# Kernel tuning notes

Hardware: AMD Instinct MI355X
Metric: run time of the kernel (lower is better)

The kernel has to match this reference:

```python
import jax, jax.numpy as jnp
import numpy as np

SQ = 1.0 / np.sqrt(2.0)

def _haar_filters():
    dec_lo = np.array([SQ, SQ], np.float32); dec_hi = np.array([-SQ, SQ], np.float32)
    rec_lo = np.array([SQ, SQ], np.float32); rec_hi = np.array([SQ, -SQ], np.float32)
    def bank(lo, hi):
        ks = []
        for fz in (lo, hi):
            for fy in (lo, hi):
                for fx in (lo, hi):
                    ks.append(np.einsum('i,j,k->ijk', fz, fy, fx))
        return jnp.asarray(np.stack(ks, 0))  # [8,2,2,2]
    return bank(dec_lo, dec_hi), bank(rec_lo, rec_hi)

WT_F, IWT_F = _haar_filters()

def dwt3(x):
    # stride-2 2x2x2 cross-correlation == reshape + einsum (kernel size == stride)
    B, C, D, H, W = x.shape
    xr = x.reshape(B, C, D // 2, 2, H // 2, 2, W // 2, 2)
    return jnp.einsum('bcdzhywx,fzyx->bcfdhw', xr, WT_F)  # [B,C,8,D/2,H/2,W/2]

def idwt3(x):
    # conv_transpose3d stride 2 kernel 2: no overlap -> einsum + reshape
    B, C, _, D, H, W = x.shape
    out = jnp.einsum('bcfdhw,fzyx->bcdzhywx', x, IWT_F)
    return out.reshape(B, C, 2 * D, 2 * H, 2 * W)

def dwconv3(x, w, b=None):
    # depthwise 3x3x3 conv, padding SAME (torch padding='same', groups=C)
    y = jax.lax.conv_general_dilated(
        x, w, (1, 1, 1), 'SAME',
        dimension_numbers=('NCDHW', 'OIDHW', 'NCDHW'),
        feature_group_count=x.shape[1])
    if b is not None:
        y = y + b[None, :, None, None, None]
    return y

WT_LEVELS = 2

def setup_inputs() -> dict:
    key = jax.random.key(0)
    ks = jax.random.split(key, 6)
    B, C, D, H, W = 1, 64, 64, 64, 64
    return {
        'x': jax.random.normal(ks[0], (B, C, D, H, W), jnp.float32),
        'base_w': jax.random.normal(ks[1], (C, 1, 3, 3, 3), jnp.float32) * 0.1,
        'base_b': jax.random.normal(ks[2], (C,), jnp.float32) * 0.02,
        'base_scale_w': jnp.ones((1, C, 1, 1, 1), jnp.float32),
        'wconv_w0': jax.random.normal(ks[3], (C * 8, 1, 3, 3, 3), jnp.float32) * 0.1,
        'wconv_w1': jax.random.normal(ks[4], (C * 8, 1, 3, 3, 3), jnp.float32) * 0.1,
        'wscale0': jnp.full((1, C * 8, 1, 1, 1), 0.1, jnp.float32),
        'wscale1': jnp.full((1, C * 8, 1, 1, 1), 0.1, jnp.float32),
        'lambd': jnp.float32(0.05),
    }

def reference(x, base_w, base_b, base_scale_w, wconv_w0, wconv_w1, wscale0, wscale1, lambd):
    wconv_ws = (wconv_w0, wconv_w1)
    wscales = (wscale0, wscale1)
    lls, hfs, shapes = [], [], []
    cur = x
    for i in range(WT_LEVELS):
        shapes.append(cur.shape)
        pd, ph, pw = cur.shape[2] % 2, cur.shape[3] % 2, cur.shape[4] % 2
        if pd or ph or pw:
            cur = jnp.pad(cur, ((0, 0), (0, 0), (0, pd), (0, ph), (0, pw)))
        cx = dwt3(cur)                     # [B,C,8,d,h,w]
        cur = cx[:, :, 0]                  # LL passes to next level
        B, C, _, d, h, w = cx.shape
        t = dwconv3(cx.reshape(B, C * 8, d, h, w), wconv_ws[i])
        t = t.reshape(B, C, 8, d, h, w)
        ll, hf = t[:, :, :1], t[:, :, 1:]
        hf = jnp.sign(hf) * jax.nn.relu(jnp.abs(hf) - lambd)  # soft threshold
        t = jnp.concatenate([ll, hf], axis=2)
        t = (t.reshape(B, C * 8, d, h, w) * wscales[i]).reshape(B, C, 8, d, h, w)
        lls.append(t[:, :, 0]); hfs.append(t[:, :, 1:])
    nxt = jnp.float32(0.0)
    for i in range(WT_LEVELS - 1, -1, -1):
        cll = lls[i] + nxt
        cx = jnp.concatenate([cll[:, :, None], hfs[i]], axis=2)
        nxt = idwt3(cx)
        sh = shapes[i]
        nxt = nxt[:, :, :sh[2], :sh[3], :sh[4]]
    base = dwconv3(x, base_w, base_b) * base_scale_w
    return base + nxt
```

## Files before the change

### kernel.cpp

```cpp
#include <hip/hip_runtime.h>

#define SQ3F 0.35355339059327379f

__device__ __forceinline__ void haar_fwd(const float v[8], float o[8]) {
    float ax[8];
#pragma unroll
    for (int i = 0; i < 4; ++i) {
        float a = v[2 * i], b = v[2 * i + 1];
        ax[2 * i]     = a + b;
        ax[2 * i + 1] = b - a;
    }
    float ay[8];
#pragma unroll
    for (int z = 0; z < 2; ++z)
#pragma unroll
        for (int bx = 0; bx < 2; ++bx) {
            float a = ax[z * 4 + bx], b = ax[z * 4 + 2 + bx];
            ay[z * 4 + bx]     = a + b;
            ay[z * 4 + 2 + bx] = b - a;
        }
#pragma unroll
    for (int j = 0; j < 4; ++j) {
        float a = ay[j], b = ay[4 + j];
        o[j]     = (a + b) * SQ3F;
        o[4 + j] = (b - a) * SQ3F;
    }
}

__device__ __forceinline__ void haar_inv(const float t[8], float o[8]) {
    float az[8];
#pragma unroll
    for (int j = 0; j < 4; ++j) {
        float lo = t[j], hi = t[4 + j];
        az[j]     = lo + hi;
        az[4 + j] = lo - hi;
    }
    float ay[8];
#pragma unroll
    for (int z = 0; z < 2; ++z)
#pragma unroll
        for (int bx = 0; bx < 2; ++bx) {
            float lo = az[z * 4 + bx], hi = az[z * 4 + 2 + bx];
            ay[z * 4 + bx]     = lo + hi;
            ay[z * 4 + 2 + bx] = lo - hi;
        }
#pragma unroll
    for (int i = 0; i < 4; ++i) {
        float lo = ay[2 * i], hi = ay[2 * i + 1];
        o[2 * i]     = (lo + hi) * SQ3F;
        o[2 * i + 1] = (lo - hi) * SQ3F;
    }
}

__global__ __launch_bounds__(512, 4) void fused_l0_k(
    const float* __restrict__ x, const float* __restrict__ wt,
    const float* __restrict__ wscale, const float* __restrict__ lambd_p,
    float* __restrict__ t0, float* __restrict__ ll) {
    __shared__ __align__(16) float pl[8][32][36];
    int bx   = blockIdx.x;
    int slab = bx & 7;
    int c    = bx >> 3;
    int z0   = slab * 4;
    int tid  = threadIdx.x;

    {
        int fi   = tid >> 6;
        int rowi = (tid >> 1) & 31;
        pl[fi][rowi][(tid & 1) * 33] = 0.f;
    }

    int f    = __builtin_amdgcn_readfirstlane(tid >> 6);
    int lane = tid & 63;
    int cty  = lane >> 1;
    int cx0i = (lane & 1) * 16;
    int cc   = c * 8 + f;
    float wv[27];
    const float* wp = wt + cc * 27;
#pragma unroll
    for (int k = 0; k < 27; ++k) wv[k] = wp[k];
    float lam = *lambd_p;
    float sc  = wscale[cc];

    const float* xc = x + ((long)c << 18);

    int y0c = tid >> 5;
    int xx0 = tid & 31;

    float2 ld[2][4];

    auto issue_loads = [&](int p) {
#pragma unroll
        for (int half = 0; half < 2; ++half) {
            int y = y0c + half * 16;
#pragma unroll
            for (int z = 0; z < 2; ++z)
#pragma unroll
                for (int yy = 0; yy < 2; ++yy)
                    ld[half][z * 2 + yy] = *(const float2*)(
                        xc + (((2 * p + z) << 6) + (2 * y + yy)) * 64 + 2 * xx0);
        }
    };
    auto stage_write = [&](int p, bool dolls) {
#pragma unroll
        for (int half = 0; half < 2; ++half) {
            int y = y0c + half * 16;
            float v[8];
            v[0] = ld[half][0].x; v[1] = ld[half][0].y;
            v[2] = ld[half][1].x; v[3] = ld[half][1].y;
            v[4] = ld[half][2].x; v[5] = ld[half][2].y;
            v[6] = ld[half][3].x; v[7] = ld[half][3].y;
            float o[8];
            haar_fwd(v, o);
#pragma unroll
            for (int k = 0; k < 8; ++k) pl[k][y][xx0 + 1] = o[k];
            if (dolls) ll[(c << 15) + (p << 10) + (y << 5) + xx0] = o[0];
        }
    };

    float acc[3][16];
#pragma unroll
    for (int s = 0; s < 3; ++s)
#pragma unroll
        for (int j = 0; j < 16; ++j) acc[s][j] = 0.f;

    {
        int p = z0 - 1;
        if (p >= 0) {
            issue_loads(p);
            stage_write(p, false);
        }
    }
    __syncthreads();

#pragma unroll
    for (int pp = 0; pp < 6; ++pp) {
        int p       = z0 - 1 + pp;
        bool pvalid = (p >= 0) && (p <= 31);
        int pn      = p + 1;
        bool pnv    = (pp < 5) && (pn <= 31);

        if (pnv) issue_loads(pn);

        if (pvalid) {
#pragma unroll
            for (int dy = 0; dy < 3; ++dy) {
                int yy = cty - 1 + dy;
                if ((unsigned)yy < 32u) {
                    float r[18];
                    {
                        const float* rp = &pl[f][yy][cx0i];
                        float4 a0 = *(const float4*)(rp);
                        float4 a1 = *(const float4*)(rp + 4);
                        float4 a2 = *(const float4*)(rp + 8);
                        float4 a3 = *(const float4*)(rp + 12);
                        float2 a4 = *(const float2*)(rp + 16);
                        r[0]  = a0.x; r[1]  = a0.y; r[2]  = a0.z; r[3]  = a0.w;
                        r[4]  = a1.x; r[5]  = a1.y; r[6]  = a1.z; r[7]  = a1.w;
                        r[8]  = a2.x; r[9]  = a2.y; r[10] = a2.z; r[11] = a2.w;
                        r[12] = a3.x; r[13] = a3.y; r[14] = a3.z; r[15] = a3.w;
                        r[16] = a4.x; r[17] = a4.y;
                    }
#pragma unroll
                    for (int dz = 0; dz < 3; ++dz) {
                        int rel = pp - dz;
                        if (rel >= 0 && rel <= 3) {
                            int s = rel % 3;
#pragma unroll
                            for (int dx = 0; dx < 3; ++dx) {
                                float wgt = wv[dz * 9 + dy * 3 + dx];
#pragma unroll
                                for (int j = 0; j < 16; ++j)
                                    acc[s][j] += r[dx + j] * wgt;
                            }
                        }
                    }
                }
            }
        }
        {
            int rel = pp - 2;
            if (rel >= 0 && rel <= 3) {
                int zc = z0 + rel;
                int s  = rel % 3;
                float res[16];
#pragma unroll
                for (int j = 0; j < 16; ++j) {
                    float t = acc[s][j];
                    if (f != 0) {
                        float a = fabsf(t) - lam;
                        t       = a > 0.f ? copysignf(a, t) : 0.f;
                    }
                    res[j]    = t * sc;
                    acc[s][j] = 0.f;
                }
                float* op = t0 + ((long)cc << 15) + (zc << 10) + cty * 32 + cx0i;
#pragma unroll
                for (int q = 0; q < 4; ++q)
                    *(float4*)(op + q * 4) = float4{res[q * 4], res[q * 4 + 1],
                                                    res[q * 4 + 2], res[q * 4 + 3]};
            }
        }
        __syncthreads();
        if (pnv) stage_write(pn, pp < 4);
        __syncthreads();
    }
}

template <int SO>
__global__ __launch_bounds__(256) void dwt3_k(const float* __restrict__ in,
                                              int inChStride,
                                              float* __restrict__ out) {
    constexpr int SI = SO * 2;
    int idx = blockIdx.x * 256 + threadIdx.x;
    int w = idx % SO;
    int h = (idx / SO) % SO;
    int d = (idx / (SO * SO)) % SO;
    int c = idx / (SO * SO * SO);
    const float* ip = in + (long)c * inChStride;
    float v[8];
#pragma unroll
    for (int z = 0; z < 2; ++z)
#pragma unroll
        for (int y = 0; y < 2; ++y) {
            const float2 p =
                *(const float2*)(ip + ((2 * d + z) * SI + (2 * h + y)) * SI + 2 * w);
            v[z * 4 + y * 2]     = p.x;
            v[z * 4 + y * 2 + 1] = p.y;
        }
    float o[8];
    haar_fwd(v, o);
    int s = (d * SO + h) * SO + w;
#pragma unroll
    for (int f = 0; f < 8; ++f) out[(c * 8 + f) * (SO * SO * SO) + s] = o[f];
}

template <int S, int PH>
__device__ __forceinline__ void conv_step(const float* __restrict__ ip, int zo,
                                          int ty, int x0,
                                          const float* __restrict__ wv,
                                          float win[3][3][6], float lam, float sc,
                                          bool hf, float* __restrict__ op) {
    constexpr int sPrev = (PH + 2) % 3;
    constexpr int sCur  = PH;
    constexpr int sNext = (PH + 1) % 3;
    {
        int zz = zo + 1;
        bool zok = zz < S;
        const float* pp = ip + zz * S * S;
#pragma unroll
        for (int dy = 0; dy < 3; ++dy) {
            int yy  = ty - 1 + dy;
            bool yok = zok && ((unsigned)yy < (unsigned)S);
            const float* rp = pp + yy * S;
            win[sNext][dy][0] = (yok && x0 > 0) ? rp[x0 - 1] : 0.f;
            float4 m = yok ? *(const float4*)(rp + x0) : float4{0.f, 0.f, 0.f, 0.f};
            win[sNext][dy][1] = m.x;
            win[sNext][dy][2] = m.y;
            win[sNext][dy][3] = m.z;
            win[sNext][dy][4] = m.w;
            win[sNext][dy][5] = (yok && (x0 + 4 < S)) ? rp[x0 + 4] : 0.f;
        }
    }
    float acc[4] = {0.f, 0.f, 0.f, 0.f};
#pragma unroll
    for (int dz = 0; dz < 3; ++dz) {
        const float(*wp)[6] = (dz == 0) ? win[sPrev] : (dz == 1) ? win[sCur] : win[sNext];
#pragma unroll
        for (int dy = 0; dy < 3; ++dy)
#pragma unroll
            for (int dx = 0; dx < 3; ++dx) {
                float wgt = wv[dz * 9 + dy * 3 + dx];
#pragma unroll
                for (int j = 0; j < 4; ++j) acc[j] += wp[dy][dx + j] * wgt;
            }
    }
    float4 r;
    float* rr = (float*)&r;
#pragma unroll
    for (int j = 0; j < 4; ++j) {
        float t = acc[j];
        if (hf) {
            float a = fabsf(t) - lam;
            t       = a > 0.f ? copysignf(a, t) : 0.f;
        }
        rr[j] = t * sc;
    }
    *(float4*)(op + (zo * S + ty) * S + x0) = r;
}

template <int S, int SLOT>
__device__ __forceinline__ void load_win_plane(const float* __restrict__ ip,
                                               int z, int ty, int x0,
                                               float win[3][3][6]) {
    bool zok = ((unsigned)z < (unsigned)S);
    const float* pp = ip + z * S * S;
#pragma unroll
    for (int dy = 0; dy < 3; ++dy) {
        int yy  = ty - 1 + dy;
        bool yok = zok && ((unsigned)yy < (unsigned)S);
        const float* rp = pp + yy * S;
        win[SLOT][dy][0] = (yok && x0 > 0) ? rp[x0 - 1] : 0.f;
        float4 m = yok ? *(const float4*)(rp + x0) : float4{0.f, 0.f, 0.f, 0.f};
        win[SLOT][dy][1] = m.x;
        win[SLOT][dy][2] = m.y;
        win[SLOT][dy][3] = m.z;
        win[SLOT][dy][4] = m.w;
        win[SLOT][dy][5] = (yok && (x0 + 4 < S)) ? rp[x0 + 4] : 0.f;
    }
}

template <int S, int PH0>
__device__ __forceinline__ void run_chunk(const float* __restrict__ ip, int z0,
                                          int ty, int x0,
                                          const float* __restrict__ wv,
                                          float win[3][3][6], float lam, float sc,
                                          bool hf, float* __restrict__ op) {
    load_win_plane<S, (PH0 + 2) % 3>(ip, z0 - 1, ty, x0, win);
    load_win_plane<S, PH0>(ip, z0, ty, x0, win);
    conv_step<S, PH0>(ip, z0, ty, x0, wv, win, lam, sc, hf, op);
    conv_step<S, (PH0 + 1) % 3>(ip, z0 + 1, ty, x0, wv, win, lam, sc, hf, op);
    conv_step<S, (PH0 + 2) % 3>(ip, z0 + 2, ty, x0, wv, win, lam, sc, hf, op);
    conv_step<S, PH0>(ip, z0 + 3, ty, x0, wv, win, lam, sc, hf, op);
}

template <int S, int CPB>
__global__ __launch_bounds__(256) void dwconv_soft_chunk_k(
    const float* __restrict__ in, const float* __restrict__ wt,
    const float* __restrict__ wscale, const float* __restrict__ lambd_p,
    float* __restrict__ out) {
    constexpr int TX = S / 4;
    int tid = threadIdx.x;
    int tx  = tid % TX;
    int ty  = (tid / TX) % S;
    int cs  = tid / (TX * S);
    int zc  = blockIdx.x & 3;
    int cg  = blockIdx.x >> 2;
    int cc  = cg * CPB + cs;
    const float* ip = in + (long)cc * (S * S * S);
    float* op       = out + (long)cc * (S * S * S);
    float wv[27];
#pragma unroll
    for (int k = 0; k < 27; ++k) wv[k] = wt[cc * 27 + k];
    float lam = *lambd_p;
    float sc  = wscale[cc];
    bool hf   = (cc & 7) != 0;
    int x0    = 4 * tx;

    float win[3][3][6];
    switch (zc) {
        case 0:  run_chunk<S, 0>(ip, 0,  ty, x0, wv, win, lam, sc, hf, op); break;
        case 1:  run_chunk<S, 1>(ip, 4,  ty, x0, wv, win, lam, sc, hf, op); break;
        case 2:  run_chunk<S, 2>(ip, 8,  ty, x0, wv, win, lam, sc, hf, op); break;
        default: run_chunk<S, 0>(ip, 12, ty, x0, wv, win, lam, sc, hf, op); break;
    }
}

__global__ __launch_bounds__(256, 3) void final_k2(
    const float* __restrict__ x, const float* __restrict__ t0,
    const float* __restrict__ t1, const float* __restrict__ bw,
    const float* __restrict__ bb, const float* __restrict__ bscale,
    float* __restrict__ out) {
    __shared__ float xs[18 * 10 * 67];
    int bx = blockIdx.x;
    int c  = bx >> 5;
    int ti = bx & 31;
    int dt = ti >> 3;
    int ht = ti & 7;
    const float* xc = x + ((long)c << 18);
    int zg0 = 16 * dt - 1, yg0 = 8 * ht - 1;
    for (int i = threadIdx.x; i < 18 * 10 * 66; i += 256) {
        int pz = i / 660;
        int r  = i - pz * 660;
        int py = r / 66;
        int px = r - py * 66;
        int zg = zg0 + pz, yg = yg0 + py, xg = px - 1;
        bool ok = ((unsigned)zg < 64u) && ((unsigned)yg < 64u) && ((unsigned)xg < 64u);
        xs[(pz * 10 + py) * 67 + px] = ok ? xc[(zg << 12) + (yg << 6) + xg] : 0.f;
    }
    const float* wp0 = bw + c * 27;
    float wv[27];
#pragma unroll
    for (int k = 0; k < 27; ++k) wv[k] = wp0[k];
    float bias = bb[c], scl = bscale[c];
    __syncthreads();

    int tid = threadIdx.x;
    int wc  = tid & 7;
    int hc  = (tid >> 3) & 3;
    int dc  = tid >> 5;
    int d   = dt * 8 + dc;
    int h   = ht * 4 + hc;
    int w0  = wc * 4;

    float acc[2][2][8];
#pragma unroll
    for (int oz = 0; oz < 2; ++oz)
#pragma unroll
        for (int oy = 0; oy < 2; ++oy)
#pragma unroll
            for (int m = 0; m < 8; ++m) acc[oz][oy][m] = 0.f;

#pragma unroll
    for (int pz = 0; pz < 4; ++pz) {
        float r[4][10];
#pragma unroll
        for (int py = 0; py < 4; ++py)
#pragma unroll
            for (int k = 0; k < 10; ++k)
                r[py][k] = xs[((2 * dc + pz) * 10 + (2 * hc + py)) * 67 + 8 * wc + k];
#pragma unroll
        for (int oz = 0; oz < 2; ++oz) {
            int kz = pz - oz;
            if (kz >= 0 && kz <= 2) {
#pragma unroll
                for (int py = 0; py < 4; ++py)
#pragma unroll
                    for (int oy = 0; oy < 2; ++oy) {
                        int ky = py - oy;
                        if (ky >= 0 && ky <= 2) {
#pragma unroll
                            for (int kx = 0; kx < 3; ++kx) {
                                float wgt = wv[kz * 9 + ky * 3 + kx];
#pragma unroll
                                for (int m = 0; m < 8; ++m)
                                    acc[oz][oy][m] += r[py][m + kx] * wgt;
                            }
                        }
                    }
            }
        }
    }

    int cell0 = (d << 10) + (h << 5) + w0;
    float4 t0v[8];
#pragma unroll
    for (int f = 0; f < 8; ++f)
        t0v[f] = *(const float4*)(t0 + (((long)(c * 8 + f)) << 15) + cell0);
    int s1b = ((d >> 1) * 16 + (h >> 1)) * 16 + (w0 >> 1);
    float2 t1v[8];
#pragma unroll
    for (int f = 0; f < 8; ++f)
        t1v[f] = *(const float2*)(t1 + ((c * 8 + f) << 12) + s1b);

#pragma unroll
    for (int j = 0; j < 4; ++j) {
        int w = w0 + j;
        float tf[8];
#pragma unroll
        for (int f = 0; f < 8; ++f) tf[f] = ((const float*)&t0v[f])[j];
        float add = 0.f;
#pragma unroll
        for (int f = 0; f < 8; ++f) {
            float v  = (j >> 1) ? t1v[f].y : t1v[f].x;
            float sg = 1.f;
            if ((f & 4) && (d & 1)) sg = -sg;
            if ((f & 2) && (h & 1)) sg = -sg;
            if ((f & 1) && (j & 1)) sg = -sg;
            add += sg * v;
        }
        tf[0] += add * SQ3F;
        float contrib[8];
        haar_inv(tf, contrib);
#pragma unroll
        for (int oz = 0; oz < 2; ++oz)
#pragma unroll
            for (int oy = 0; oy < 2; ++oy) {
                float2 rr;
                rr.x = (acc[oz][oy][2 * j] + bias) * scl + contrib[oz * 4 + oy * 2];
                rr.y = (acc[oz][oy][2 * j + 1] + bias) * scl +
                       contrib[oz * 4 + oy * 2 + 1];
                *(float2*)(out + ((long)c << 18) + ((2 * d + oz) << 12) +
                           ((2 * h + oy) << 6) + 2 * w) = rr;
            }
    }
}

extern "C" void kernel_launch(void* const* d_in, const int* in_sizes, int n_in,
                              void* d_out, int out_size, void* d_ws, size_t ws_size,
                              hipStream_t stream) {
    const float* x      = (const float*)d_in[0];
    const float* base_w = (const float*)d_in[1];
    const float* base_b = (const float*)d_in[2];
    const float* base_s = (const float*)d_in[3];
    const float* w0     = (const float*)d_in[4];
    const float* w1     = (const float*)d_in[5];
    const float* ws0    = (const float*)d_in[6];
    const float* ws1    = (const float*)d_in[7];
    const float* lambd  = (const float*)d_in[8];
    float* out = (float*)d_out;

    float* ll  = (float*)d_ws;
    float* t0  = ll + 2097152;
    float* cx1 = t0 + 16777216;
    float* t1  = cx1 + 2097152;

    fused_l0_k<<<512, 512, 0, stream>>>(x, w0, ws0, lambd, t0, ll);
    dwt3_k<16><<<1024, 256, 0, stream>>>(ll, 32768, cx1);
    dwconv_soft_chunk_k<16, 4><<<512, 256, 0, stream>>>(cx1, w1, ws1, lambd, t1);
    final_k2<<<2048, 256, 0, stream>>>(x, t0, t1, base_w, base_b, base_s, out);
}
```

Before: 259.0 us.

## Drop level-0 prefetch pipeline and double threads in final fused kernel

In the fused level-0 kernel, the register-prefetch software pipeline is replaced by a simpler per-plane load of float4s. Each thread now transforms two adjacent Haar cells and stores LL as float2, with one sync on each side. The final kernel moves from 256 to 512 threads per block, halving per-thread output width, and now writes contiguous float4 rows. It also broadcasts the uniform weights with readfirstlane to keep them in scalar registers. The intent is more parallelism, lower register pressure and wider stores, at the cost of losing load/compute overlap in the level-0 kernel and recomputing more halo reads per thread.

```diff
diff --git a/kernel.cpp b/kernel.cpp
--- a/kernel.cpp
+++ b/kernel.cpp
@@ -1,6 +1,10 @@
 #include <hip/hip_runtime.h>
 
 #define SQ3F 0.35355339059327379f
+
+__device__ __forceinline__ float rfl(float v) {
+    return __int_as_float(__builtin_amdgcn_readfirstlane(__float_as_int(v)));
+}
 
 __device__ __forceinline__ void haar_fwd(const float v[8], float o[8]) {
     float ax[8];
@@ -83,64 +87,46 @@
 
     const float* xc = x + ((long)c << 18);
 
-    int y0c = tid >> 5;
-    int xx0 = tid & 31;
-
-    float2 ld[2][4];
-
-    auto issue_loads = [&](int p) {
-#pragma unroll
-        for (int half = 0; half < 2; ++half) {
-            int y = y0c + half * 16;
-#pragma unroll
-            for (int z = 0; z < 2; ++z)
-#pragma unroll
-                for (int yy = 0; yy < 2; ++yy)
-                    ld[half][z * 2 + yy] = *(const float2*)(
-                        xc + (((2 * p + z) << 6) + (2 * y + yy)) * 64 + 2 * xx0);
-        }
-    };
-    auto stage_write = [&](int p, bool dolls) {
-#pragma unroll
-        for (int half = 0; half < 2; ++half) {
-            int y = y0c + half * 16;
-            float v[8];
-            v[0] = ld[half][0].x; v[1] = ld[half][0].y;
-            v[2] = ld[half][1].x; v[3] = ld[half][1].y;
-            v[4] = ld[half][2].x; v[5] = ld[half][2].y;
-            v[6] = ld[half][3].x; v[7] = ld[half][3].y;
-            float o[8];
-            haar_fwd(v, o);
-#pragma unroll
-            for (int k = 0; k < 8; ++k) pl[k][y][xx0 + 1] = o[k];
-            if (dolls) ll[(c << 15) + (p << 10) + (y << 5) + xx0] = o[0];
-        }
-    };
-
     float acc[3][16];
 #pragma unroll
     for (int s = 0; s < 3; ++s)
 #pragma unroll
         for (int j = 0; j < 16; ++j) acc[s][j] = 0.f;
-
-    {
-        int p = z0 - 1;
-        if (p >= 0) {
-            issue_loads(p);
-            stage_write(p, false);
-        }
-    }
-    __syncthreads();
 
 #pragma unroll
     for (int pp = 0; pp < 6; ++pp) {
         int p       = z0 - 1 + pp;
         bool pvalid = (p >= 0) && (p <= 31);
-        int pn      = p + 1;
-        bool pnv    = (pp < 5) && (pn <= 31);
-
-        if (pnv) issue_loads(pn);
-
+        __syncthreads();
+        if (pvalid) {
+            int cell = 2 * tid;
+            int y    = cell >> 5;
+            int xx   = cell & 31;
+            float v0[8], v1[8];
+#pragma unroll
+            for (int z = 0; z < 2; ++z)
+#pragma unroll
+                for (int yy = 0; yy < 2; ++yy) {
+                    float4 q = *(const float4*)(xc + (((2 * p + z) << 6) +
+                                                      (2 * y + yy)) * 64 + 2 * xx);
+                    v0[z * 4 + yy * 2]     = q.x;
+                    v0[z * 4 + yy * 2 + 1] = q.y;
+                    v1[z * 4 + yy * 2]     = q.z;
+                    v1[z * 4 + yy * 2 + 1] = q.w;
+                }
+            float o0[8], o1[8];
+            haar_fwd(v0, o0);
+            haar_fwd(v1, o1);
+#pragma unroll
+            for (int k = 0; k < 8; ++k) {
+                pl[k][y][xx + 1] = o0[k];
+                pl[k][y][xx + 2] = o1[k];
+            }
+            if (pp >= 1 && pp <= 4)
+                *(float2*)(ll + (c << 15) + (p << 10) + cell) =
+                    float2{o0[0], o1[0]};
+        }
+        __syncthreads();
         if (pvalid) {
 #pragma unroll
             for (int dy = 0; dy < 3; ++dy) {
@@ -200,9 +186,6 @@
                                                     res[q * 4 + 2], res[q * 4 + 3]};
             }
         }
-        __syncthreads();
-        if (pnv) stage_write(pn, pp < 4);
-        __syncthreads();
     }
 }
 
@@ -355,7 +338,7 @@
     }
 }
 
-__global__ __launch_bounds__(256, 3) void final_k2(
+__global__ __launch_bounds__(512, 6) void final_k2w(
     const float* __restrict__ x, const float* __restrict__ t0,
     const float* __restrict__ t1, const float* __restrict__ bw,
     const float* __restrict__ bb, const float* __restrict__ bscale,
@@ -368,7 +351,7 @@
     int ht = ti & 7;
     const float* xc = x + ((long)c << 18);
     int zg0 = 16 * dt - 1, yg0 = 8 * ht - 1;
-    for (int i = threadIdx.x; i < 18 * 10 * 66; i += 256) {
+    for (int i = threadIdx.x; i < 18 * 10 * 66; i += 512) {
         int pz = i / 660;
         int r  = i - pz * 660;
         int py = r / 66;
@@ -380,34 +363,34 @@
     const float* wp0 = bw + c * 27;
     float wv[27];
 #pragma unroll
-    for (int k = 0; k < 27; ++k) wv[k] = wp0[k];
-    float bias = bb[c], scl = bscale[c];
+    for (int k = 0; k < 27; ++k) wv[k] = rfl(wp0[k]);
+    float bias = rfl(bb[c]), scl = rfl(bscale[c]);
     __syncthreads();
 
     int tid = threadIdx.x;
-    int wc  = tid & 7;
-    int hc  = (tid >> 3) & 3;
-    int dc  = tid >> 5;
+    int wc  = tid & 15;
+    int hc  = (tid >> 4) & 3;
+    int dc  = tid >> 6;
     int d   = dt * 8 + dc;
     int h   = ht * 4 + hc;
-    int w0  = wc * 4;
-
-    float acc[2][2][8];
+    int x0  = wc * 4;
+
+    float acc[2][2][4];
 #pragma unroll
     for (int oz = 0; oz < 2; ++oz)
 #pragma unroll
         for (int oy = 0; oy < 2; ++oy)
 #pragma unroll
-            for (int m = 0; m < 8; ++m) acc[oz][oy][m] = 0.f;
+            for (int m = 0; m < 4; ++m) acc[oz][oy][m] = 0.f;
 
 #pragma unroll
     for (int pz = 0; pz < 4; ++pz) {
-        float r[4][10];
+        float r[4][6];
 #pragma unroll
         for (int py = 0; py < 4; ++py)
 #pragma unroll
-            for (int k = 0; k < 10; ++k)
-                r[py][k] = xs[((2 * dc + pz) * 10 + (2 * hc + py)) * 67 + 8 * wc + k];
+            for (int k = 0; k < 6; ++k)
+                r[py][k] = xs[((2 * dc + pz) * 10 + (2 * hc + py)) * 67 + 4 * wc + k];
 #pragma unroll
         for (int oz = 0; oz < 2; ++oz) {
             int kz = pz - oz;
@@ -422,7 +405,7 @@
                             for (int kx = 0; kx < 3; ++kx) {
                                 float wgt = wv[kz * 9 + ky * 3 + kx];
 #pragma unroll
-                                for (int m = 0; m < 8; ++m)
+                                for (int m = 0; m < 4; ++m)
                                     acc[oz][oy][m] += r[py][m + kx] * wgt;
                             }
                         }
@@ -431,48 +414,48 @@
         }
     }
 
-    int cell0 = (d << 10) + (h << 5) + w0;
-    float4 t0v[8];
+    int cell0 = (d << 10) + (h << 5) + 2 * wc;
+    float2 t0v[8];
 #pragma unroll
     for (int f = 0; f < 8; ++f)
-        t0v[f] = *(const float4*)(t0 + (((long)(c * 8 + f)) << 15) + cell0);
-    int s1b = ((d >> 1) * 16 + (h >> 1)) * 16 + (w0 >> 1);
-    float2 t1v[8];
+        t0v[f] = *(const float2*)(t0 + (((long)(c * 8 + f)) << 15) + cell0);
+    int s1b = ((d >> 1) * 16 + (h >> 1)) * 16 + wc;
+    float t1v[8];
 #pragma unroll
     for (int f = 0; f < 8; ++f)
-        t1v[f] = *(const float2*)(t1 + ((c * 8 + f) << 12) + s1b);
-
-#pragma unroll
-    for (int j = 0; j < 4; ++j) {
-        int w = w0 + j;
+        t1v[f] = t1[((c * 8 + f) << 12) + s1b];
+
+    float c0[8], c1[8];
+#pragma unroll
+    for (int j = 0; j < 2; ++j) {
         float tf[8];
 #pragma unroll
-        for (int f = 0; f < 8; ++f) tf[f] = ((const float*)&t0v[f])[j];
+        for (int f = 0; f < 8; ++f) tf[f] = j ? t0v[f].y : t0v[f].x;
         float add = 0.f;
 #pragma unroll
         for (int f = 0; f < 8; ++f) {
-            float v  = (j >> 1) ? t1v[f].y : t1v[f].x;
             float sg = 1.f;
             if ((f & 4) && (d & 1)) sg = -sg;
             if ((f & 2) && (h & 1)) sg = -sg;
-            if ((f & 1) && (j & 1)) sg = -sg;
-            add += sg * v;
+            if ((f & 1) && j) sg = -sg;
+            add += sg * t1v[f];
         }
         tf[0] += add * SQ3F;
-        float contrib[8];
-        haar_inv(tf, contrib);
-#pragma unroll
-        for (int oz = 0; oz < 2; ++oz)
-#pragma unroll
-            for (int oy = 0; oy < 2; ++oy) {
-                float2 rr;
-                rr.x = (acc[oz][oy][2 * j] + bias) * scl + contrib[oz * 4 + oy * 2];
-                rr.y = (acc[oz][oy][2 * j + 1] + bias) * scl +
-                       contrib[oz * 4 + oy * 2 + 1];
-                *(float2*)(out + ((long)c << 18) + ((2 * d + oz) << 12) +
-                           ((2 * h + oy) << 6) + 2 * w) = rr;
-            }
-    }
+        haar_inv(tf, j ? c1 : c0);
+    }
+
+#pragma unroll
+    for (int oz = 0; oz < 2; ++oz)
+#pragma unroll
+        for (int oy = 0; oy < 2; ++oy) {
+            float4 rv;
+            rv.x = (acc[oz][oy][0] + bias) * scl + c0[oz * 4 + oy * 2];
+            rv.y = (acc[oz][oy][1] + bias) * scl + c0[oz * 4 + oy * 2 + 1];
+            rv.z = (acc[oz][oy][2] + bias) * scl + c1[oz * 4 + oy * 2];
+            rv.w = (acc[oz][oy][3] + bias) * scl + c1[oz * 4 + oy * 2 + 1];
+            *(float4*)(out + ((long)c << 18) + ((2 * d + oz) << 12) +
+                       ((2 * h + oy) << 6) + x0) = rv;
+        }
 }
 
 extern "C" void kernel_launch(void* const* d_in, const int* in_sizes, int n_in,
@@ -497,5 +480,5 @@
     fused_l0_k<<<512, 512, 0, stream>>>(x, w0, ws0, lambd, t0, ll);
     dwt3_k<16><<<1024, 256, 0, stream>>>(ll, 32768, cx1);
     dwconv_soft_chunk_k<16, 4><<<512, 256, 0, stream>>>(cx1, w1, ws1, lambd, t1);
-    final_k2<<<2048, 256, 0, stream>>>(x, t0, t1, base_w, base_b, base_s, out);
-}
+    final_k2w<<<2048, 512, 0, stream>>>(x, t0, t1, base_w, base_b, base_s, out);
+}
```

Result: slower. 298.9 us (+15.4%).

## Halve per-block depth slab in fused level-0 kernel, drop register prefetch

Applied to the files above, without the earlier changes.

Each block of the fused level-0 DWT and depthwise-conv kernel now covers 2 output depth planes instead of 4, so the grid doubles to 1024 blocks and the accumulator ring shrinks from 3 to 2 slots. The register double-buffered prefetch is replaced by a synchronous load, Haar transform and LDS store at the top of each iteration, using float4 loads that cover two cells per thread. Weights and scalars are forced into scalar registers via readfirstlane, and launch bounds ask for 6 blocks per CU. This aims to raise occupancy and cut register pressure, but it re-reads more halo planes per output plane (4 input planes for 2 outputs) and no longer overlaps global loads with compute.

```diff
diff --git a/kernel.cpp b/kernel.cpp
--- a/kernel.cpp
+++ b/kernel.cpp
@@ -1,6 +1,10 @@
 #include <hip/hip_runtime.h>
 
 #define SQ3F 0.35355339059327379f
+
+__device__ __forceinline__ float rfl(float v) {
+    return __int_as_float(__builtin_amdgcn_readfirstlane(__float_as_int(v)));
+}
 
 __device__ __forceinline__ void haar_fwd(const float v[8], float o[8]) {
     float ax[8];
@@ -52,15 +56,15 @@
     }
 }
 
-__global__ __launch_bounds__(512, 4) void fused_l0_k(
+__global__ __launch_bounds__(512, 6) void fused_l0_k(
     const float* __restrict__ x, const float* __restrict__ wt,
     const float* __restrict__ wscale, const float* __restrict__ lambd_p,
     float* __restrict__ t0, float* __restrict__ ll) {
     __shared__ __align__(16) float pl[8][32][36];
     int bx   = blockIdx.x;
-    int slab = bx & 7;
-    int c    = bx >> 3;
-    int z0   = slab * 4;
+    int slab = bx & 15;
+    int c    = bx >> 4;
+    int z0   = slab * 2;
     int tid  = threadIdx.x;
 
     {
@@ -77,70 +81,52 @@
     float wv[27];
     const float* wp = wt + cc * 27;
 #pragma unroll
-    for (int k = 0; k < 27; ++k) wv[k] = wp[k];
-    float lam = *lambd_p;
-    float sc  = wscale[cc];
+    for (int k = 0; k < 27; ++k) wv[k] = rfl(wp[k]);
+    float lam = rfl(*lambd_p);
+    float sc  = rfl(wscale[cc]);
 
     const float* xc = x + ((long)c << 18);
 
-    int y0c = tid >> 5;
-    int xx0 = tid & 31;
-
-    float2 ld[2][4];
-
-    auto issue_loads = [&](int p) {
-#pragma unroll
-        for (int half = 0; half < 2; ++half) {
-            int y = y0c + half * 16;
-#pragma unroll
-            for (int z = 0; z < 2; ++z)
-#pragma unroll
-                for (int yy = 0; yy < 2; ++yy)
-                    ld[half][z * 2 + yy] = *(const float2*)(
-                        xc + (((2 * p + z) << 6) + (2 * y + yy)) * 64 + 2 * xx0);
-        }
-    };
-    auto stage_write = [&](int p, bool dolls) {
-#pragma unroll
-        for (int half = 0; half < 2; ++half) {
-            int y = y0c + half * 16;
-            float v[8];
-            v[0] = ld[half][0].x; v[1] = ld[half][0].y;
-            v[2] = ld[half][1].x; v[3] = ld[half][1].y;
-            v[4] = ld[half][2].x; v[5] = ld[half][2].y;
-            v[6] = ld[half][3].x; v[7] = ld[half][3].y;
-            float o[8];
-            haar_fwd(v, o);
-#pragma unroll
-            for (int k = 0; k < 8; ++k) pl[k][y][xx0 + 1] = o[k];
-            if (dolls) ll[(c << 15) + (p << 10) + (y << 5) + xx0] = o[0];
-        }
-    };
-
-    float acc[3][16];
-#pragma unroll
-    for (int s = 0; s < 3; ++s)
+    float acc[2][16];
+#pragma unroll
+    for (int s = 0; s < 2; ++s)
 #pragma unroll
         for (int j = 0; j < 16; ++j) acc[s][j] = 0.f;
 
-    {
-        int p = z0 - 1;
-        if (p >= 0) {
-            issue_loads(p);
-            stage_write(p, false);
-        }
-    }
-    __syncthreads();
-
-#pragma unroll
-    for (int pp = 0; pp < 6; ++pp) {
+#pragma unroll
+    for (int pp = 0; pp < 4; ++pp) {
         int p       = z0 - 1 + pp;
         bool pvalid = (p >= 0) && (p <= 31);
-        int pn      = p + 1;
-        bool pnv    = (pp < 5) && (pn <= 31);
-
-        if (pnv) issue_loads(pn);
-
+        __syncthreads();
+        if (pvalid) {
+            int cell = 2 * tid;
+            int y    = cell >> 5;
+            int xx   = cell & 31;
+            float v0[8], v1[8];
+#pragma unroll
+            for (int z = 0; z < 2; ++z)
+#pragma unroll
+                for (int yy = 0; yy < 2; ++yy) {
+                    float4 q = *(const float4*)(xc + (((2 * p + z) << 6) +
+                                                      (2 * y + yy)) * 64 + 2 * xx);
+                    v0[z * 4 + yy * 2]     = q.x;
+                    v0[z * 4 + yy * 2 + 1] = q.y;
+                    v1[z * 4 + yy * 2]     = q.z;
+                    v1[z * 4 + yy * 2 + 1] = q.w;
+                }
+            float o0[8], o1[8];
+            haar_fwd(v0, o0);
+            haar_fwd(v1, o1);
+#pragma unroll
+            for (int k = 0; k < 8; ++k) {
+                pl[k][y][xx + 1] = o0[k];
+                pl[k][y][xx + 2] = o1[k];
+            }
+            if (pp == 1 || pp == 2)
+                *(float2*)(ll + (c << 15) + (p << 10) + cell) =
+                    float2{o0[0], o1[0]};
+        }
+        __syncthreads();
         if (pvalid) {
 #pragma unroll
             for (int dy = 0; dy < 3; ++dy) {
@@ -163,14 +149,13 @@
 #pragma unroll
                     for (int dz = 0; dz < 3; ++dz) {
                         int rel = pp - dz;
-                        if (rel >= 0 && rel <= 3) {
-                            int s = rel % 3;
+                        if (rel >= 0 && rel <= 1) {
 #pragma unroll
                             for (int dx = 0; dx < 3; ++dx) {
                                 float wgt = wv[dz * 9 + dy * 3 + dx];
 #pragma unroll
                                 for (int j = 0; j < 16; ++j)
-                                    acc[s][j] += r[dx + j] * wgt;
+                                    acc[rel][j] += r[dx + j] * wgt;
                             }
                         }
                     }
@@ -179,19 +164,18 @@
         }
         {
             int rel = pp - 2;
-            if (rel >= 0 && rel <= 3) {
+            if (rel >= 0 && rel <= 1) {
                 int zc = z0 + rel;
-                int s  = rel % 3;
                 float res[16];
 #pragma unroll
                 for (int j = 0; j < 16; ++j) {
-                    float t = acc[s][j];
+                    float t = acc[rel][j];
                     if (f != 0) {
                         float a = fabsf(t) - lam;
                         t       = a > 0.f ? copysignf(a, t) : 0.f;
                     }
-                    res[j]    = t * sc;
-                    acc[s][j] = 0.f;
+                    res[j]      = t * sc;
+                    acc[rel][j] = 0.f;
                 }
                 float* op = t0 + ((long)cc << 15) + (zc << 10) + cty * 32 + cx0i;
 #pragma unroll
@@ -200,9 +184,6 @@
                                                     res[q * 4 + 2], res[q * 4 + 3]};
             }
         }
-        __syncthreads();
-        if (pnv) stage_write(pn, pp < 4);
-        __syncthreads();
     }
 }
 
@@ -494,7 +475,7 @@
     float* cx1 = t0 + 16777216;
     float* t1  = cx1 + 2097152;
 
-    fused_l0_k<<<512, 512, 0, stream>>>(x, w0, ws0, lambd, t0, ll);
+    fused_l0_k<<<1024, 512, 0, stream>>>(x, w0, ws0, lambd, t0, ll);
     dwt3_k<16><<<1024, 256, 0, stream>>>(ll, 32768, cx1);
     dwconv_soft_chunk_k<16, 4><<<512, 256, 0, stream>>>(cx1, w1, ws1, lambd, t1);
     final_k2<<<2048, 256, 0, stream>>>(x, t0, t1, base_w, base_b, base_s, out);
```

After: 251.4 us. 1.03x faster.
